# Kernel tuning notes

Hardware: AMD Instinct MI355X
Metric: run time of the kernel (lower is better)

The kernel has to match this reference:

```python
import jax, jax.numpy as jnp
import numpy as np

R = 16
ALPHA = 32
SCALING = ALPHA / R
SLOTS = 32
IN_F = 4096
OUT_F = 4096
B, T = 8, 1024


def setup_inputs() -> dict:
    key = jax.random.key(0)
    k1, k2, k3, k4, k5, k6 = jax.random.split(key, 6)
    x = jax.random.normal(k1, (B, T, IN_F), dtype=jnp.float32)
    adapter_mapping = jax.random.randint(k2, (B,), 0, SLOTS, dtype=jnp.int32)
    W = jax.random.normal(k3, (OUT_F, IN_F), dtype=jnp.float32) * 0.02
    b = jax.random.normal(k4, (OUT_F,), dtype=jnp.float32) * 0.02
    lora_As = jax.random.normal(k5, (SLOTS, IN_F, R), dtype=jnp.float32) * 0.02
    lora_Bs = jax.random.normal(k6, (SLOTS, R, OUT_F), dtype=jnp.float32) * 0.02
    return {"x": x, "adapter_mapping": adapter_mapping, "W": W, "b": b,
            "lora_As": lora_As, "lora_Bs": lora_Bs}


def reference(x, adapter_mapping, W, b, lora_As, lora_Bs):
    # base linear: y = x @ W.T + b
    base_out = jnp.einsum('bti,oi->bto', x, W) + b
    # per-example adapter gather (index_select along slot dim)
    A = lora_As[adapter_mapping]          # [B, in, r]
    Bm = lora_Bs[adapter_mapping]         # [B, r, out]
    lora_h = jnp.einsum('bti,bir->btr', x, A)
    lora_out = jnp.einsum('btr,bro->bto', lora_h, Bm)
    return base_out + lora_out * SCALING
```

## Files before the change

### kernel.cpp

```cpp
#include <hip/hip_runtime.h>
#include <hip/hip_bf16.h>


typedef __bf16 bf16_t;
typedef __bf16 bf16x8 __attribute__((ext_vector_type(8)));
typedef __bf16 bf16x4 __attribute__((ext_vector_type(4)));
typedef float f32x4 __attribute__((ext_vector_type(4)));

#define M_DIM 8192
#define K_DIM 4096
#define N_DIM 4096
#define SCALE_F 2.0f
#define NT (K_DIM / 64)

__device__ __forceinline__ void gload_lds16(const void* g, void* l) {
    __builtin_amdgcn_global_load_lds(
        (const __attribute__((address_space(1))) void*)g,
        (__attribute__((address_space(3))) void*)l, 16, 0, 0);
}

__global__ __launch_bounds__(256) void cvt_kernel(const float* __restrict__ src,
                                                  bf16_t* __restrict__ dst, int n4) {
    int i = blockIdx.x * 256 + threadIdx.x;
    const int stride = gridDim.x * 256;
    for (; i < n4; i += stride) {
        f32x4 v = ((const f32x4*)src)[i];
        bf16x4 o = {(bf16_t)v[0], (bf16_t)v[1], (bf16_t)v[2], (bf16_t)v[3]};
        ((bf16x4*)dst)[i] = o;
    }
}

__global__ __launch_bounds__(256) void lora_hx_kernel(
    const float* __restrict__ X,
    const float* __restrict__ lora_As,
    const int* __restrict__ mapping,
    float* __restrict__ h_ws,
    bf16_t* __restrict__ Xb)
{
    __shared__ bf16_t Xt[32 * 16 * 8];
    __shared__ bf16_t At[16 * 136];
    __shared__ float hred[4 * 2 * 16 * 16];

    const int tid  = threadIdx.x;
    const int wave = tid >> 6;
    const int lane = tid & 63;
    const int bm0  = blockIdx.x * 32;
    const int slot = mapping[bm0 >> 10];
    const float* __restrict__ A = lora_As + (size_t)slot * (K_DIM * 16);

    const int srow = tid >> 3;
    const int sc2  = tid & 7;
    const int r16  = lane & 15;
    const int kq   = lane >> 4;

    f32x4 acc[2];
    acc[0] = (f32x4){0.f, 0.f, 0.f, 0.f};
    acc[1] = (f32x4){0.f, 0.f, 0.f, 0.f};

    for (int k0 = 0; k0 < K_DIM; k0 += 128) {
        const float* xp = X + (size_t)(bm0 + srow) * K_DIM + k0 + sc2 * 16;
        f32x4 v0 = *(const f32x4*)(xp);
        f32x4 v1 = *(const f32x4*)(xp + 4);
        f32x4 v2 = *(const f32x4*)(xp + 8);
        f32x4 v3 = *(const f32x4*)(xp + 12);
        bf16x8 c0 = {(bf16_t)v0[0], (bf16_t)v0[1], (bf16_t)v0[2], (bf16_t)v0[3],
                     (bf16_t)v1[0], (bf16_t)v1[1], (bf16_t)v1[2], (bf16_t)v1[3]};
        bf16x8 c1 = {(bf16_t)v2[0], (bf16_t)v2[1], (bf16_t)v2[2], (bf16_t)v2[3],
                     (bf16_t)v3[0], (bf16_t)v3[1], (bf16_t)v3[2], (bf16_t)v3[3]};
        if (Xb) {
            bf16x8* xbp = (bf16x8*)(Xb + (size_t)(bm0 + srow) * K_DIM + k0 + sc2 * 16);
            xbp[0] = c0;
            xbp[1] = c1;
        }
        const int k8a = sc2 * 2, k8b = sc2 * 2 + 1;
        *(bf16x8*)(Xt + (srow * 16 + (k8a ^ (srow & 15))) * 8) = c0;
        *(bf16x8*)(Xt + (srow * 16 + (k8b ^ (srow & 15))) * 8) = c1;

        {
            const int kk = tid >> 1, half = tid & 1;
            const float* ap = A + (size_t)(k0 + kk) * 16 + half * 8;
            f32x4 a0 = *(const f32x4*)ap;
            f32x4 a1 = *(const f32x4*)(ap + 4);
#pragma unroll
            for (int rr = 0; rr < 4; ++rr) {
                At[(half * 8 + rr) * 136 + kk]     = (bf16_t)a0[rr];
                At[(half * 8 + 4 + rr) * 136 + kk] = (bf16_t)a1[rr];
            }
        }
        __syncthreads();

#pragma unroll
        for (int i = 0; i < 2; ++i) {
            const int row_l = i * 16 + r16;
            const int c = wave * 4 + kq;
            bf16x8 af  = *(const bf16x8*)(Xt + (row_l * 16 + (c ^ (row_l & 15))) * 8);
            bf16x8 bfr = *(const bf16x8*)(At + r16 * 136 + wave * 32 + kq * 8);
            acc[i] = __builtin_amdgcn_mfma_f32_16x16x32_bf16(af, bfr, acc[i], 0, 0, 0);
        }
        __syncthreads();
    }

#pragma unroll
    for (int i = 0; i < 2; ++i)
#pragma unroll
        for (int e = 0; e < 4; ++e)
            hred[wave * 512 + i * 256 + (kq * 4 + e) * 16 + r16] = acc[i][e];
    __syncthreads();
#pragma unroll
    for (int q = 0; q < 2; ++q) {
        const int entry = tid * 2 + q;
        const int row_l = entry >> 4, col = entry & 15;
        const int i = row_l >> 4, rr = row_l & 15;
        const int off = i * 256 + rr * 16 + col;
        float s = hred[off] + hred[512 + off] + hred[1024 + off] + hred[1536 + off];
        h_ws[(size_t)(bm0 + row_l) * 16 + col] = s * SCALE_F;
    }
}

__device__ __forceinline__ void epilogue(
    f32x4 (&acc)[4][4], const float* __restrict__ bias,
    const float* __restrict__ lora_Bs, const int* __restrict__ mapping,
    const float* __restrict__ h_ws, float* __restrict__ out,
    int bm0, int bn0, int wm0, int wn0, int r16, int kq)
{
    const int slot = mapping[bm0 >> 10];
    const bool hasK = (kq < 2);
    const int kq2 = hasK ? kq : 0;

    bf16x8 hfrag[4], bmf[4];
#pragma unroll
    for (int i = 0; i < 4; ++i) {
        const float* hp = h_ws + (size_t)(bm0 + wm0 + i * 16 + r16) * 16 + kq2 * 8;
        f32x4 h0 = *(const f32x4*)hp;
        f32x4 h1 = *(const f32x4*)(hp + 4);
#pragma unroll
        for (int jj = 0; jj < 4; ++jj) {
            hfrag[i][jj]     = hasK ? (bf16_t)h0[jj] : (bf16_t)0.f;
            hfrag[i][jj + 4] = hasK ? (bf16_t)h1[jj] : (bf16_t)0.f;
        }
    }
#pragma unroll
    for (int j = 0; j < 4; ++j) {
        const int o = bn0 + wn0 + j * 16 + r16;
#pragma unroll
        for (int jj = 0; jj < 8; ++jj) {
            const int r = kq2 * 8 + jj;
            const float v = lora_Bs[((size_t)slot * 16 + r) * N_DIM + o];
            bmf[j][jj] = hasK ? (bf16_t)v : (bf16_t)0.f;
        }
    }
#pragma unroll
    for (int i = 0; i < 4; ++i)
#pragma unroll
        for (int j = 0; j < 4; ++j)
            acc[i][j] = __builtin_amdgcn_mfma_f32_16x16x32_bf16(hfrag[i], bmf[j], acc[i][j], 0, 0, 0);

#pragma unroll
    for (int j = 0; j < 4; ++j) {
        const int o = bn0 + wn0 + j * 16 + r16;
        const float bv = bias[o];
#pragma unroll
        for (int i = 0; i < 4; ++i) {
#pragma unroll
            for (int e = 0; e < 4; ++e) {
                const int m = bm0 + wm0 + i * 16 + kq * 4 + e;
                out[(size_t)m * N_DIM + o] = acc[i][j][e] + bv;
            }
        }
    }
}

__device__ __forceinline__ void stage256(const bf16_t* __restrict__ G, int grow0, int k0,
                                         bf16_t* lds, int wave, int lane) {
#pragma unroll
    for (int p = 0; p < 4; ++p) {
        const int base = p * 512 + wave * 64;
        const int s    = base + lane;
        const int row  = s >> 3;
        const int c    = (s & 7) ^ (row & 7);
        gload_lds16(G + (size_t)(grow0 + row) * K_DIM + k0 + c * 8,
                    lds + (size_t)base * 8);
    }
}

__global__ __launch_bounds__(512, 2) void gemm_lora_256(
    const bf16_t* __restrict__ Xb, const bf16_t* __restrict__ Wb,
    const float* __restrict__ bias, const float* __restrict__ lora_Bs,
    const int* __restrict__ mapping, const float* __restrict__ h_ws,
    float* __restrict__ out)
{
    __shared__ bf16_t As[2][256 * 64];
    __shared__ bf16_t Bs[2][256 * 64];

    const int tid  = threadIdx.x;
    const int wave = tid >> 6;
    const int lane = tid & 63;
    const int bid  = blockIdx.x;
    const int wgid = (bid & 7) * 64 + (bid >> 3);
    const int m_t  = wgid >> 4;
    const int n_t  = wgid & 15;
    const int bm0  = m_t * 256;
    const int bn0  = n_t * 256;
    const int wr   = wave >> 2;
    const int wc   = wave & 3;
    const int r16  = lane & 15;
    const int kq   = lane >> 4;

    f32x4 acc[8][4];
#pragma unroll
    for (int i = 0; i < 8; ++i)
#pragma unroll
        for (int j = 0; j < 4; ++j) acc[i][j] = (f32x4){0.f, 0.f, 0.f, 0.f};

    stage256(Xb, bm0, 0, As[0], wave, lane);
    stage256(Wb, bn0, 0, Bs[0], wave, lane);
    asm volatile("s_waitcnt vmcnt(0)" ::: "memory");
    __builtin_amdgcn_s_barrier();

#pragma unroll 2
    for (int t = 0; t < NT; ++t) {
        const int b = t & 1;
        const bf16_t* Ab = As[b];
        const bf16_t* Bb = Bs[b];
        bf16_t* An = As[b ^ 1];
        bf16_t* Bn = Bs[b ^ 1];
        const bool pre = (t + 1 < NT);
        const int k0n  = (t + 1) * 64;

        bf16x8 af[4], bfr[4];

#pragma unroll
        for (int i = 0; i < 4; ++i) {
            const int ra = wr * 128 + i * 16 + r16;
            af[i] = *(const bf16x8*)(Ab + ((size_t)ra * 8 + (kq ^ (ra & 7))) * 8);
        }
#pragma unroll
        for (int j = 0; j < 4; ++j) {
            const int rb = wc * 64 + j * 16 + r16;
            bfr[j] = *(const bf16x8*)(Bb + ((size_t)rb * 8 + (kq ^ (rb & 7))) * 8);
        }
        if (pre) stage256(Xb, bm0, k0n, An, wave, lane);
        __builtin_amdgcn_s_barrier();
        __builtin_amdgcn_s_setprio(1);
#pragma unroll
        for (int i = 0; i < 4; ++i)
#pragma unroll
            for (int j = 0; j < 4; ++j)
                acc[i][j] = __builtin_amdgcn_mfma_f32_16x16x32_bf16(af[i], bfr[j], acc[i][j], 0, 0, 0);
        __builtin_amdgcn_s_setprio(0);
        __builtin_amdgcn_s_barrier();

#pragma unroll
        for (int i = 0; i < 4; ++i) {
            const int ra = wr * 128 + 64 + i * 16 + r16;
            af[i] = *(const bf16x8*)(Ab + ((size_t)ra * 8 + (kq ^ (ra & 7))) * 8);
        }
        if (pre) stage256(Wb, bn0, k0n, Bn, wave, lane);
        __builtin_amdgcn_s_barrier();
        __builtin_amdgcn_s_setprio(1);
#pragma unroll
        for (int i = 0; i < 4; ++i)
#pragma unroll
            for (int j = 0; j < 4; ++j)
                acc[4 + i][j] = __builtin_amdgcn_mfma_f32_16x16x32_bf16(af[i], bfr[j], acc[4 + i][j], 0, 0, 0);
        __builtin_amdgcn_s_setprio(0);
        __builtin_amdgcn_s_barrier();

#pragma unroll
        for (int i = 0; i < 4; ++i) {
            const int ra = wr * 128 + i * 16 + r16;
            af[i] = *(const bf16x8*)(Ab + ((size_t)ra * 8 + ((4 + kq) ^ (ra & 7))) * 8);
        }
#pragma unroll
        for (int j = 0; j < 4; ++j) {
            const int rb = wc * 64 + j * 16 + r16;
            bfr[j] = *(const bf16x8*)(Bb + ((size_t)rb * 8 + ((4 + kq) ^ (rb & 7))) * 8);
        }
        __builtin_amdgcn_s_barrier();
        __builtin_amdgcn_s_setprio(1);
#pragma unroll
        for (int i = 0; i < 4; ++i)
#pragma unroll
            for (int j = 0; j < 4; ++j)
                acc[i][j] = __builtin_amdgcn_mfma_f32_16x16x32_bf16(af[i], bfr[j], acc[i][j], 0, 0, 0);
        __builtin_amdgcn_s_setprio(0);
        __builtin_amdgcn_s_barrier();

#pragma unroll
        for (int i = 0; i < 4; ++i) {
            const int ra = wr * 128 + 64 + i * 16 + r16;
            af[i] = *(const bf16x8*)(Ab + ((size_t)ra * 8 + ((4 + kq) ^ (ra & 7))) * 8);
        }
        __builtin_amdgcn_s_barrier();
        __builtin_amdgcn_s_setprio(1);
#pragma unroll
        for (int i = 0; i < 4; ++i)
#pragma unroll
            for (int j = 0; j < 4; ++j)
                acc[4 + i][j] = __builtin_amdgcn_mfma_f32_16x16x32_bf16(af[i], bfr[j], acc[4 + i][j], 0, 0, 0);
        __builtin_amdgcn_s_setprio(0);
        if (pre) {
            asm volatile("s_waitcnt vmcnt(0)" ::: "memory");
        }
        __builtin_amdgcn_s_barrier();
    }

    const int slot = mapping[bm0 >> 10];
    const bool hasK = (kq < 2);
    const int kq2 = hasK ? kq : 0;
    const int wm0 = wr * 128, wn0 = wc * 64;

    bf16x8 hfrag[8], bmf[4];
#pragma unroll
    for (int i = 0; i < 8; ++i) {
        const float* hp = h_ws + (size_t)(bm0 + wm0 + i * 16 + r16) * 16 + kq2 * 8;
        f32x4 h0 = *(const f32x4*)hp;
        f32x4 h1 = *(const f32x4*)(hp + 4);
#pragma unroll
        for (int jj = 0; jj < 4; ++jj) {
            hfrag[i][jj]     = hasK ? (bf16_t)h0[jj] : (bf16_t)0.f;
            hfrag[i][jj + 4] = hasK ? (bf16_t)h1[jj] : (bf16_t)0.f;
        }
    }
#pragma unroll
    for (int j = 0; j < 4; ++j) {
        const int o = bn0 + wn0 + j * 16 + r16;
#pragma unroll
        for (int jj = 0; jj < 8; ++jj) {
            const int r = kq2 * 8 + jj;
            const float v = lora_Bs[((size_t)slot * 16 + r) * N_DIM + o];
            bmf[j][jj] = hasK ? (bf16_t)v : (bf16_t)0.f;
        }
    }
#pragma unroll
    for (int i = 0; i < 8; ++i)
#pragma unroll
        for (int j = 0; j < 4; ++j)
            acc[i][j] = __builtin_amdgcn_mfma_f32_16x16x32_bf16(hfrag[i], bmf[j], acc[i][j], 0, 0, 0);

#pragma unroll
    for (int j = 0; j < 4; ++j) {
        const int o = bn0 + wn0 + j * 16 + r16;
        const float bv = bias[o];
#pragma unroll
        for (int i = 0; i < 8; ++i) {
#pragma unroll
            for (int e = 0; e < 4; ++e) {
                const int m = bm0 + wm0 + i * 16 + kq * 4 + e;
                out[(size_t)m * N_DIM + o] = acc[i][j][e] + bv;
            }
        }
    }
}

__global__ __launch_bounds__(256) void gemm_lora_f32s(
    const float* __restrict__ Xf, const float* __restrict__ Wf,
    const float* __restrict__ bias, const float* __restrict__ lora_Bs,
    const int* __restrict__ mapping, const float* __restrict__ h_ws,
    float* __restrict__ out)
{
    __shared__ float Asf[128 * 32];
    __shared__ float Bsf[128 * 32];

    const int tid  = threadIdx.x;
    const int wave = tid >> 6;
    const int lane = tid & 63;
    const int bid  = blockIdx.x;
    const int n_t  = (bid & 7) + ((bid >> 9) << 3);
    const int m_t  = (bid >> 3) & 63;
    const int bm0 = m_t * 128;
    const int bn0 = n_t * 128;
    const int wm0 = (wave >> 1) * 64;
    const int wn0 = (wave & 1) * 64;
    const int r16 = lane & 15;
    const int kq  = lane >> 4;

    f32x4 acc[4][4];
#pragma unroll
    for (int i = 0; i < 4; ++i)
#pragma unroll
        for (int j = 0; j < 4; ++j) acc[i][j] = (f32x4){0.f, 0.f, 0.f, 0.f};

    for (int k0 = 0; k0 < K_DIM; k0 += 32) {
#pragma unroll
        for (int p = 0; p < 4; ++p) {
            const int idx0 = (p * 4 + wave) * 64;
            const int idx  = idx0 + lane;
            const int k4   = idx >> 7;
            const int row  = idx & 127;
            gload_lds16(Xf + (size_t)(bm0 + row) * K_DIM + (k0 + k4 * 4),
                        Asf + (size_t)idx0 * 4);
            gload_lds16(Wf + (size_t)(bn0 + row) * K_DIM + (k0 + k4 * 4),
                        Bsf + (size_t)idx0 * 4);
        }
        __syncthreads();

        bf16x8 af[4], bfr[4];
#pragma unroll
        for (int i = 0; i < 4; ++i) {
            const int ra = wm0 + i * 16 + r16;
            const int rb = wn0 + i * 16 + r16;
            f32x4 a0 = *(const f32x4*)(Asf + ((size_t)(kq * 2) * 128 + ra) * 4);
            f32x4 a1 = *(const f32x4*)(Asf + ((size_t)(kq * 2 + 1) * 128 + ra) * 4);
            f32x4 b0 = *(const f32x4*)(Bsf + ((size_t)(kq * 2) * 128 + rb) * 4);
            f32x4 b1 = *(const f32x4*)(Bsf + ((size_t)(kq * 2 + 1) * 128 + rb) * 4);
            af[i]  = (bf16x8){(bf16_t)a0[0], (bf16_t)a0[1], (bf16_t)a0[2], (bf16_t)a0[3],
                              (bf16_t)a1[0], (bf16_t)a1[1], (bf16_t)a1[2], (bf16_t)a1[3]};
            bfr[i] = (bf16x8){(bf16_t)b0[0], (bf16_t)b0[1], (bf16_t)b0[2], (bf16_t)b0[3],
                              (bf16_t)b1[0], (bf16_t)b1[1], (bf16_t)b1[2], (bf16_t)b1[3]};
        }
#pragma unroll
        for (int i = 0; i < 4; ++i)
#pragma unroll
            for (int j = 0; j < 4; ++j)
                acc[i][j] = __builtin_amdgcn_mfma_f32_16x16x32_bf16(af[i], bfr[j], acc[i][j], 0, 0, 0);
        __syncthreads();
    }

    epilogue(acc, bias, lora_Bs, mapping, h_ws, out, bm0, bn0, wm0, wn0, r16, kq);
}

extern "C" void kernel_launch(void* const* d_in, const int* in_sizes, int n_in,
                              void* d_out, int out_size, void* d_ws, size_t ws_size,
                              hipStream_t stream) {
    const float* x        = (const float*)d_in[0];
    const int*   mapping  = (const int*)d_in[1];
    const float* W        = (const float*)d_in[2];
    const float* b        = (const float*)d_in[3];
    const float* lora_As  = (const float*)d_in[4];
    const float* lora_Bs  = (const float*)d_in[5];
    float* out = (float*)d_out;

    const size_t xb_bytes = (size_t)M_DIM * K_DIM * 2;
    const size_t wb_bytes = (size_t)N_DIM * K_DIM * 2;
    const size_t h_bytes  = (size_t)M_DIM * 16 * 4;
    const bool direct = ws_size >= xb_bytes + wb_bytes + h_bytes;

    bf16_t* Xb = (bf16_t*)d_ws;
    bf16_t* Wb = (bf16_t*)((char*)d_ws + xb_bytes);
    float*  h_ws = direct ? (float*)((char*)d_ws + xb_bytes + wb_bytes)
                          : (float*)d_ws;

    lora_hx_kernel<<<dim3(M_DIM / 32), 256, 0, stream>>>(
        x, lora_As, mapping, h_ws, direct ? Xb : nullptr);

    if (direct) {
        cvt_kernel<<<dim3(2048), 256, 0, stream>>>(W, Wb, N_DIM * K_DIM / 4);
        gemm_lora_256<<<dim3((M_DIM / 256) * (N_DIM / 256)), 512, 0, stream>>>(
            Xb, Wb, b, lora_Bs, mapping, h_ws, out);
    } else {
        gemm_lora_f32s<<<dim3(2048), 256, 0, stream>>>(
            x, W, b, lora_Bs, mapping, h_ws, out);
    }
}
```

Baseline: 681.4 us.

## Prefetch X tile two iterations ahead with partial vmcnt waits

Restructures the double-buffered main loop so the X tile is loaded two k-steps ahead, into the buffer just finished being read, and the W tile one step ahead split across two phases. The end-of-iteration wait now leaves the four newest loads (the X prefetch) in flight instead of draining all loads. The aim is to hide more global-load latency behind the MFMA work. This relies on exact vmcnt accounting and an lgkmcnt(0) wait before overwriting the current A buffer, which makes buffer reuse races easy to introduce.

```diff
diff --git a/kernel.cpp b/kernel.cpp
--- a/kernel.cpp
+++ b/kernel.cpp
@@ -170,11 +170,11 @@
     }
 }
 
-__device__ __forceinline__ void stage256(const bf16_t* __restrict__ G, int grow0, int k0,
-                                         bf16_t* lds, int wave, int lane) {
-#pragma unroll
-    for (int p = 0; p < 4; ++p) {
-        const int base = p * 512 + wave * 64;
+__device__ __forceinline__ void stage_half(const bf16_t* __restrict__ G, int grow0, int k0,
+                                           bf16_t* lds, int part, int wave, int lane) {
+#pragma unroll
+    for (int q = 0; q < 2; ++q) {
+        const int base = part * 1024 + q * 512 + wave * 64;
         const int s    = base + lane;
         const int row  = s >> 3;
         const int c    = (s & 7) ^ (row & 7);
@@ -212,9 +212,13 @@
 #pragma unroll
         for (int j = 0; j < 4; ++j) acc[i][j] = (f32x4){0.f, 0.f, 0.f, 0.f};
 
-    stage256(Xb, bm0, 0, As[0], wave, lane);
-    stage256(Wb, bn0, 0, Bs[0], wave, lane);
-    asm volatile("s_waitcnt vmcnt(0)" ::: "memory");
+    stage_half(Xb, bm0, 0, As[0], 0, wave, lane);
+    stage_half(Xb, bm0, 0, As[0], 1, wave, lane);
+    stage_half(Wb, bn0, 0, Bs[0], 0, wave, lane);
+    stage_half(Wb, bn0, 0, Bs[0], 1, wave, lane);
+    stage_half(Xb, bm0, 64, As[1], 0, wave, lane);
+    stage_half(Xb, bm0, 64, As[1], 1, wave, lane);
+    asm volatile("s_waitcnt vmcnt(4)" ::: "memory");
     __builtin_amdgcn_s_barrier();
 
 #pragma unroll 2
@@ -222,10 +226,12 @@
         const int b = t & 1;
         const bf16_t* Ab = As[b];
         const bf16_t* Bb = Bs[b];
-        bf16_t* An = As[b ^ 1];
-        bf16_t* Bn = Bs[b ^ 1];
-        const bool pre = (t + 1 < NT);
-        const int k0n  = (t + 1) * 64;
+        bf16_t* Bnx = Bs[b ^ 1];
+        bf16_t* Aff = As[b];
+        const bool pre1 = (t + 1 < NT);
+        const bool pre2 = (t + 2 < NT);
+        const int k1 = (t + 1) * 64;
+        const int k2 = (t + 2) * 64;
 
         bf16x8 af[4], bfr[4];
 
@@ -239,7 +245,7 @@
             const int rb = wc * 64 + j * 16 + r16;
             bfr[j] = *(const bf16x8*)(Bb + ((size_t)rb * 8 + (kq ^ (rb & 7))) * 8);
         }
-        if (pre) stage256(Xb, bm0, k0n, An, wave, lane);
+        if (pre1) stage_half(Wb, bn0, k1, Bnx, 0, wave, lane);
         __builtin_amdgcn_s_barrier();
         __builtin_amdgcn_s_setprio(1);
 #pragma unroll
@@ -255,7 +261,7 @@
             const int ra = wr * 128 + 64 + i * 16 + r16;
             af[i] = *(const bf16x8*)(Ab + ((size_t)ra * 8 + (kq ^ (ra & 7))) * 8);
         }
-        if (pre) stage256(Wb, bn0, k0n, Bn, wave, lane);
+        if (pre1) stage_half(Wb, bn0, k1, Bnx, 1, wave, lane);
         __builtin_amdgcn_s_barrier();
         __builtin_amdgcn_s_setprio(1);
 #pragma unroll
@@ -291,7 +297,14 @@
             const int ra = wr * 128 + 64 + i * 16 + r16;
             af[i] = *(const bf16x8*)(Ab + ((size_t)ra * 8 + ((4 + kq) ^ (ra & 7))) * 8);
         }
-        __builtin_amdgcn_s_barrier();
+        __builtin_amdgcn_sched_barrier(0);
+        asm volatile("s_waitcnt lgkmcnt(0)" ::: "memory");
+        __builtin_amdgcn_sched_barrier(0);
+        __builtin_amdgcn_s_barrier();
+        if (pre2) {
+            stage_half(Xb, bm0, k2, Aff, 0, wave, lane);
+            stage_half(Xb, bm0, k2, Aff, 1, wave, lane);
+        }
         __builtin_amdgcn_s_setprio(1);
 #pragma unroll
         for (int i = 0; i < 4; ++i)
@@ -299,8 +312,9 @@
             for (int j = 0; j < 4; ++j)
                 acc[4 + i][j] = __builtin_amdgcn_mfma_f32_16x16x32_bf16(af[i], bfr[j], acc[4 + i][j], 0, 0, 0);
         __builtin_amdgcn_s_setprio(0);
-        if (pre) {
-            asm volatile("s_waitcnt vmcnt(0)" ::: "memory");
+        if (pre1) {
+            if (pre2) asm volatile("s_waitcnt vmcnt(4)" ::: "memory");
+            else      asm volatile("s_waitcnt vmcnt(0)" ::: "memory");
         }
         __builtin_amdgcn_s_barrier();
     }
```

New measurement: 705.6 us. 1.04x slower.
